# Kernel optimization log

Hardware: AMD Instinct MI355X
Metric: run time of the kernel (lower is better)

Reference implementation:

```python
import jax, jax.numpy as jnp
import numpy as np
from jax import lax

B, C, W, H = 32, 64, 32, 32
HEADS, RED = 4, 16
D = C // HEADS


def setup_inputs() -> dict:
    key = jax.random.key(0)
    ks = jax.random.split(key, 16)
    s = 0.05
    return {
        "x": jax.random.normal(ks[0], (B, C, W, H), jnp.float32),
        "Wq": jax.random.normal(ks[1], (C, C), jnp.float32) * s,
        "bq": jnp.zeros((C,), jnp.float32),
        "Wk": jax.random.normal(ks[2], (C, C), jnp.float32) * s,
        "bk": jnp.zeros((C,), jnp.float32),
        "Wv": jax.random.normal(ks[3], (C, C), jnp.float32) * s,
        "bv": jnp.zeros((C,), jnp.float32),
        "rel_h": jax.random.normal(ks[4], (1, HEADS, D, 1, H), jnp.float32),
        "rel_w": jax.random.normal(ks[5], (1, HEADS, D, W, 1), jnp.float32),
        "ln_g": jnp.ones((C, W, H), jnp.float32),
        "ln_b": jnp.zeros((C, W, H), jnp.float32),
        "ca_w1": jax.random.normal(ks[6], (C // RED, C), jnp.float32) * s,
        "ca_b1": jnp.zeros((C // RED,), jnp.float32),
        "ca_w2": jax.random.normal(ks[7], (C, C // RED), jnp.float32) * s,
        "ca_b2": jnp.zeros((C,), jnp.float32),
        "sa_w": jax.random.normal(ks[8], (1, 2, 7, 7), jnp.float32) * s,
        "sa_b": jnp.zeros((1,), jnp.float32),
    }


def reference(x, Wq, bq, Wk, bk, Wv, bv, rel_h, rel_w, ln_g, ln_b,
              ca_w1, ca_b1, ca_w2, ca_b2, sa_w, sa_b):
    b, c, w, h = x.shape
    n = w * h
    d = c // HEADS

    def conv1x1(t, wt, bt):
        return jnp.einsum('bchw,oc->bohw', t, wt) + bt[None, :, None, None]

    # ---- MHSA branch ----
    q = conv1x1(x, Wq, bq).reshape(b, HEADS, d, n)
    k = conv1x1(x, Wk, bk).reshape(b, HEADS, d, n)
    v = conv1x1(x, Wv, bv).reshape(b, HEADS, d, n)
    cc = jnp.einsum('bhdi,bhdj->bhij', q, k)                  # content-content
    pos = (rel_h + rel_w).reshape(1, HEADS, d, n)              # [1,H,d,N]
    cp = jnp.einsum('zhdi,bhdj->bhij', pos, q)                 # content-position
    att = jax.nn.softmax(cc + cp, axis=-1)                     # [b,H,N,N]
    out = jnp.einsum('bhdj,bhij->bhdi', v, att).reshape(b, c, w, h)
    # LayerNorm over (C,W,H)
    mu = jnp.mean(out, axis=(1, 2, 3), keepdims=True)
    var = jnp.var(out, axis=(1, 2, 3), keepdims=True)
    ln = (out - mu) * lax.rsqrt(var + 1e-5) * ln_g[None] + ln_b[None]
    mhsa = ln + x

    # ---- CBAM branch ----
    avg = jnp.mean(x, axis=(2, 3))                             # [b,c]
    mx = jnp.max(x, axis=(2, 3))

    def mlp(f):
        hid = jax.nn.relu(jnp.einsum('bc,oc->bo', f, ca_w1) + ca_b1)
        return jnp.einsum('bc,oc->bo', hid, ca_w2) + ca_b2

    ch_att = jax.nn.sigmoid(mlp(avg) + mlp(mx))[:, :, None, None]
    xc = ch_att * x
    feat = jnp.stack([jnp.mean(xc, axis=1), jnp.max(xc, axis=1)], axis=1)  # [b,2,w,h]
    sp = lax.conv_general_dilated(feat, sa_w, (1, 1), 'SAME',
                                  dimension_numbers=('NCHW', 'OIHW', 'NCHW'))
    sp = sp + sa_b[None, :, None, None]
    cbam = jax.nn.sigmoid(sp) * xc

    return mhsa + cbam + x
```

## Files before the change

### kernel.cpp

```cpp
#include <hip/hip_runtime.h>

#define BB 32
#define CC 64
#define WW 32
#define HHT 32
#define NH 4
#define DHD 16
#define NN 1024
#define LOG2E 1.4426950408889634f

typedef __attribute__((ext_vector_type(8))) short bf16x8;
typedef __attribute__((ext_vector_type(4))) float f32x4;

__device__ __forceinline__ float wave_sum(float v) {
#pragma unroll
  for (int off = 32; off > 0; off >>= 1) v += __shfl_down(v, off, 64);
  return v;
}
__device__ __forceinline__ float wave_max(float v) {
#pragma unroll
  for (int off = 32; off > 0; off >>= 1) v = fmaxf(v, __shfl_down(v, off, 64));
  return v;
}
__device__ __forceinline__ unsigned bf16pair(float lo, float hi) {
  unsigned a = __float_as_uint(lo), b = __float_as_uint(hi);
  a += 0x7FFFu + ((a >> 16) & 1u);
  b += 0x7FFFu + ((b >> 16) & 1u);
  return (a >> 16) | (b & 0xFFFF0000u);
}
__device__ __forceinline__ short bf16s(float f) {
  unsigned a = __float_as_uint(f);
  a += 0x7FFFu + ((a >> 16) & 1u);
  return (short)(a >> 16);
}

__global__ __launch_bounds__(256) void qkv_kernel(
    const float* __restrict__ x,
    const float* __restrict__ Wq, const float* __restrict__ bq,
    const float* __restrict__ Wk, const float* __restrict__ bk,
    const float* __restrict__ Wv, const float* __restrict__ bv,
    short* __restrict__ KQ, short* __restrict__ Vb, float* __restrict__ lnzero)
{
  __shared__ __align__(16) short Ws[192 * 72];
  const int tid = threadIdx.x;
  const int b = blockIdx.y, nt = blockIdx.x;

  if (tid < 192) {
    const int m = tid >> 4, dd = tid & 15;
    const int mat = m >> 2, h = m & 3;
    const float* src = (mat == 0 ? Wk : (mat == 1 ? Wq : Wv)) + (h * 16 + dd) * CC;
    const float scale = (mat == 0) ? LOG2E : 1.f;
    short* dst = Ws + tid * 72;
#pragma unroll
    for (int c8 = 0; c8 < 8; ++c8) {
      const float4 f0 = *reinterpret_cast<const float4*>(src + c8 * 8);
      const float4 f1 = *reinterpret_cast<const float4*>(src + c8 * 8 + 4);
      uint4 u;
      u.x = bf16pair(f0.x*scale, f0.y*scale); u.y = bf16pair(f0.z*scale, f0.w*scale);
      u.z = bf16pair(f1.x*scale, f1.y*scale); u.w = bf16pair(f1.z*scale, f1.w*scale);
      *reinterpret_cast<uint4*>(dst + c8 * 8) = u;
    }
  }
  if (blockIdx.x == 0 && blockIdx.y == 0 && tid < 64) lnzero[tid] = 0.f;
  __syncthreads();

  const int wid = tid >> 6, lane = tid & 63, Q = lane >> 4, il = lane & 15;
  const int n = nt * 64 + wid * 16 + il;
  const float* xb = x + (size_t)b * CC * NN;

  union { bf16x8 s; unsigned u[4]; } bfr[2];
#pragma unroll
  for (int half = 0; half < 2; ++half) {
#pragma unroll
    for (int p = 0; p < 4; ++p) {
      const int c0 = 32 * half + 8 * Q + 2 * p;
      const float f0 = xb[(size_t)c0 * NN + n];
      const float f1 = xb[(size_t)(c0 + 1) * NN + n];
      bfr[half].u[p] = bf16pair(f0, f1);
    }
  }

  const f32x4 zero4 = {0.f, 0.f, 0.f, 0.f};
  f32x4 acc[12];
#pragma unroll
  for (int m = 0; m < 12; ++m) {
    const short* wr = Ws + (m * 16 + il) * 72;
    const bf16x8 a0 = *reinterpret_cast<const bf16x8*>(wr + 8 * Q);
    const bf16x8 a1 = *reinterpret_cast<const bf16x8*>(wr + 32 + 8 * Q);
    acc[m] = __builtin_amdgcn_mfma_f32_16x16x32_bf16(a0, bfr[0].s, zero4, 0, 0, 0);
    acc[m] = __builtin_amdgcn_mfma_f32_16x16x32_bf16(a1, bfr[1].s, acc[m], 0, 0, 0);
  }

#pragma unroll
  for (int m = 0; m < 12; ++m) {
    const int mat = m >> 2, h = m & 3;
    const float bsc = (mat == 0) ? LOG2E : 1.f;
    const float4 bias = *reinterpret_cast<const float4*>(
        (mat == 0 ? bk : (mat == 1 ? bq : bv)) + h * 16 + 4 * Q);
    const float v0 = acc[m][0] + bias.x*bsc, v1 = acc[m][1] + bias.y*bsc;
    const float v2 = acc[m][2] + bias.z*bsc, v3 = acc[m][3] + bias.w*bsc;
    if (mat < 2) {
      uint2 pk;
      pk.x = bf16pair(v0, v1); pk.y = bf16pair(v2, v3);
      *reinterpret_cast<uint2*>(KQ + ((size_t)(b * NH + h) * NN + n) * 32 +
                                (mat == 0 ? 0 : 16) + 4 * Q) = pk;
    } else {
      short* vb = Vb + ((size_t)(b * NH + h) * 16 + 4 * Q) * NN + n;
      vb[0]            = bf16s(v0);
      vb[(size_t)NN]   = bf16s(v1);
      vb[2*(size_t)NN] = bf16s(v2);
      vb[3*(size_t)NN] = bf16s(v3);
    }
  }
}

__global__ __launch_bounds__(256, 4) void flash_kernel(
    const short* __restrict__ KQ, const short* __restrict__ Vb,
    const float* __restrict__ rel_h, const float* __restrict__ rel_w,
    float* __restrict__ attnout, float* __restrict__ lnsum, float* __restrict__ lnsum2)
{
  const int tid = threadIdx.x;
  const int wid = tid >> 6, lane = tid & 63;
  const int Q = lane >> 4, il = lane & 15;
  const int bh = blockIdx.x;
  const int h = bh & 3, b = bh >> 2;
  const int pr = wid & 1;
  const int jh = wid >> 1;
  const int ibase = blockIdx.y * 128 + pr * 64;
  const int j0base = jh * 512;

  bf16x8 bfrag[4];
#pragma unroll
  for (int g2 = 0; g2 < 4; ++g2) {
    const int i = ibase + g2*16 + il;
    if (Q < 2) {
      bfrag[g2] = *reinterpret_cast<const bf16x8*>(KQ + ((size_t)bh*NN + i)*32 + 16 + 8*Q);
    } else {
      const int wrow = i >> 5, hcol = i & 31;
      union { bf16x8 s; unsigned u[4]; } t;
#pragma unroll
      for (int p = 0; p < 4; ++p) {
        const int d0 = 8*(Q-2) + 2*p;
        const float f0 = LOG2E*(rel_h[(h*DHD + d0)*HHT + hcol] + rel_w[(h*DHD + d0)*WW + wrow]);
        const float f1 = LOG2E*(rel_h[(h*DHD + d0+1)*HHT + hcol] + rel_w[(h*DHD + d0+1)*WW + wrow]);
        t.u[p] = bf16pair(f0, f1);
      }
      bfrag[g2] = t.s;
    }
  }

  const short* KQb = KQ + (size_t)bh*NN*32;
  const short* Vbb = Vb + ((size_t)bh*16 + il)*NN;
  const f32x4 zero4 = {0.f, 0.f, 0.f, 0.f};
  f32x4 acc[4]  = {zero4, zero4, zero4, zero4};
  f32x4 lacc[4] = {zero4, zero4, zero4, zero4};
  union { bf16x8 s; unsigned u[4]; } ones;
  ones.u[0] = ones.u[1] = ones.u[2] = ones.u[3] = 0x3F803F80u;

#pragma unroll 2
  for (int t = 0; t < 8; ++t) {
    const int j0 = j0base + t*64;
    bf16x8 ag[4];
#pragma unroll
    for (int g = 0; g < 4; ++g)
      ag[g] = *reinterpret_cast<const bf16x8*>(KQb + (size_t)(j0 + 16*g + il)*32 + 8*Q);
    union { bf16x8 s; unsigned u[4]; } bv0, bv1;
    {
      const short* vp0 = Vbb + j0 + 4*Q;
      const uint2 l0 = *reinterpret_cast<const uint2*>(vp0);
      const uint2 h0 = *reinterpret_cast<const uint2*>(vp0 + 16);
      const uint2 l1 = *reinterpret_cast<const uint2*>(vp0 + 32);
      const uint2 h1 = *reinterpret_cast<const uint2*>(vp0 + 48);
      bv0.u[0] = l0.x; bv0.u[1] = l0.y; bv0.u[2] = h0.x; bv0.u[3] = h0.y;
      bv1.u[0] = l1.x; bv1.u[1] = l1.y; bv1.u[2] = h1.x; bv1.u[3] = h1.y;
    }

#pragma unroll
    for (int g2 = 0; g2 < 4; ++g2) {
      unsigned pk[4][2];
#pragma unroll
      for (int g = 0; g < 4; ++g) {
        const f32x4 s = __builtin_amdgcn_mfma_f32_16x16x32_bf16(ag[g], bfrag[g2], zero4, 0, 0, 0);
        const float p0 = __builtin_amdgcn_exp2f(s[0]);
        const float p1 = __builtin_amdgcn_exp2f(s[1]);
        const float p2 = __builtin_amdgcn_exp2f(s[2]);
        const float p3 = __builtin_amdgcn_exp2f(s[3]);
        pk[g][0] = bf16pair(p0, p1);
        pk[g][1] = bf16pair(p2, p3);
      }
#pragma unroll
      for (int hh = 0; hh < 2; ++hh) {
        union { bf16x8 s; unsigned u[4]; } ap;
        ap.u[0] = pk[2*hh][0];   ap.u[1] = pk[2*hh][1];
        ap.u[2] = pk[2*hh+1][0]; ap.u[3] = pk[2*hh+1][1];
        acc[g2]  = __builtin_amdgcn_mfma_f32_16x16x32_bf16(ap.s, hh ? bv1.s : bv0.s, acc[g2], 0, 0, 0);
        lacc[g2] = __builtin_amdgcn_mfma_f32_16x16x32_bf16(ap.s, ones.s, lacc[g2], 0, 0, 0);
      }
    }
  }

  __shared__ float cmb[2][32][64];
  __shared__ float r1[2], r2[2];
  if (jh == 1) {
#pragma unroll
    for (int g2 = 0; g2 < 4; ++g2)
#pragma unroll
      for (int r = 0; r < 4; ++r) {
        cmb[pr][g2*4 + r][lane]      = acc[g2][r];
        cmb[pr][16 + g2*4 + r][lane] = lacc[g2][r];
      }
  }
  __syncthreads();
  if (jh == 0) {
    float s1 = 0.f, s2 = 0.f;
#pragma unroll
    for (int g2 = 0; g2 < 4; ++g2)
#pragma unroll
      for (int r = 0; r < 4; ++r) {
        const float num = acc[g2][r]  + cmb[pr][g2*4 + r][lane];
        const float den = lacc[g2][r] + cmb[pr][16 + g2*4 + r][lane];
        const float v = num / den;
        const int ig = ibase + g2*16 + 4*Q + r;
        attnout[((size_t)b*CC + h*DHD + il)*NN + ig] = v;
        s1 += v; s2 += v*v;
      }
    s1 = wave_sum(s1); s2 = wave_sum(s2);
    if (lane == 0) { r1[pr] = s1; r2[pr] = s2; }
  }
  __syncthreads();
  if (tid == 0) {
    atomicAdd(&lnsum[b],  r1[0] + r1[1]);
    atomicAdd(&lnsum2[b], r2[0] + r2[1]);
  }
}

__global__ __launch_bounds__(256) void cbamstats_kernel(
    const float* __restrict__ x, float* __restrict__ avg, float* __restrict__ mx)
{
  const int bc = blockIdx.x, tid = threadIdx.x;
  const float* p = x + (size_t)bc*NN;
  float s = 0.f, m = -3.0e38f;
  for (int u = tid; u < NN; u += 256) { const float v = p[u]; s += v; m = fmaxf(m, v); }
  s = wave_sum(s); m = wave_max(m);
  __shared__ float rs[4], rm[4];
  const int wid = tid >> 6, lane = tid & 63;
  if (lane == 0) { rs[wid] = s; rm[wid] = m; }
  __syncthreads();
  if (tid == 0) {
    avg[bc] = (rs[0]+rs[1]+rs[2]+rs[3]) * (1.f/NN);
    mx[bc]  = fmaxf(fmaxf(rm[0], rm[1]), fmaxf(rm[2], rm[3]));
  }
}

__global__ __launch_bounds__(256) void mlpfeat_kernel(
    const float* __restrict__ x, const float* __restrict__ avg, const float* __restrict__ mxv,
    const float* __restrict__ w1, const float* __restrict__ b1,
    const float* __restrict__ w2, const float* __restrict__ b2,
    float* __restrict__ chv, float* __restrict__ feat)
{
  const int b = blockIdx.y, qq = blockIdx.x, tid = threadIdx.x;
  __shared__ float sa[CC], sm[CC], sch[CC];
  __shared__ float ps[4][64], pm[4][64];
  if (tid < CC) { sa[tid] = avg[b*CC + tid]; sm[tid] = mxv[b*CC + tid]; }
  __syncthreads();
  if (tid < CC) {
    float s = 2.f * b2[tid];
#pragma unroll
    for (int o = 0; o < 4; ++o) {
      float ha = b1[o], hm = b1[o];
#pragma unroll
      for (int k = 0; k < CC; ++k) { ha += w1[o*CC + k]*sa[k]; hm += w1[o*CC + k]*sm[k]; }
      s += w2[tid*4 + o] * (fmaxf(ha, 0.f) + fmaxf(hm, 0.f));
    }
    const float c = 1.f/(1.f + __expf(-s));
    sch[tid] = c;
    if (qq == 0) chv[b*CC + tid] = c;
  }
  __syncthreads();
  const int nl = tid & 63, cg = tid >> 6;
  const int n = qq*64 + nl;
  float s = 0.f, m = -3.0e38f;
#pragma unroll
  for (int c = cg*16; c < cg*16 + 16; ++c) {
    const float v = sch[c] * x[((size_t)b*CC + c)*NN + n];
    s += v; m = fmaxf(m, v);
  }
  ps[cg][nl] = s; pm[cg][nl] = m;
  __syncthreads();
  if (cg == 0) {
    const float S = ps[0][nl]+ps[1][nl]+ps[2][nl]+ps[3][nl];
    const float M = fmaxf(fmaxf(pm[0][nl], pm[1][nl]), fmaxf(pm[2][nl], pm[3][nl]));
    feat[(size_t)b*2*NN + n]      = S * (1.f/CC);
    feat[(size_t)b*2*NN + NN + n] = M;
  }
}

__global__ __launch_bounds__(256) void final_kernel(
    const float* __restrict__ x, const float* __restrict__ attn,
    const float* __restrict__ ln_g, const float* __restrict__ ln_b,
    const float* __restrict__ feat, const float* __restrict__ ch,
    const float* __restrict__ lnsum, const float* __restrict__ lnsum2,
    const float* __restrict__ sa_w, const float* __restrict__ sa_b,
    float* __restrict__ out)
{
  const int b = blockIdx.y;
  const int c0 = blockIdx.z * 16;
  const int n = blockIdx.x*256 + threadIdx.x;
  const int w = n >> 5, hh = n & 31;
  __shared__ float sch[CC];
  __shared__ float swt[98];
  if (threadIdx.x < CC) sch[threadIdx.x] = ch[b*CC + threadIdx.x];
  if (threadIdx.x < 98) swt[threadIdx.x] = sa_w[threadIdx.x];
  __syncthreads();

  float s = sa_b[0];
#pragma unroll
  for (int ci = 0; ci < 2; ++ci)
#pragma unroll
    for (int kh = 0; kh < 7; ++kh) {
      const int wy = w + kh - 3;
      if (wy < 0 || wy >= WW) continue;
#pragma unroll
      for (int kw = 0; kw < 7; ++kw) {
        const int hx = hh + kw - 3;
        if (hx < 0 || hx >= HHT) continue;
        s += feat[((size_t)(b*2) + ci)*NN + wy*HHT + hx] * swt[ci*49 + kh*7 + kw];
      }
    }
  const float sg = 1.f/(1.f + __expf(-s));
  const float inv = 1.f/(CC*NN);
  const float m = lnsum[b]*inv;
  const float var = lnsum2[b]*inv - m*m;
  const float r = rsqrtf(var + 1e-5f);
#pragma unroll
  for (int c = c0; c < c0 + 16; ++c) {
    const size_t idx = ((size_t)b*CC + c)*NN + n;
    const float xa = x[idx];
    const float ln = (attn[idx] - m) * r * ln_g[c*NN + n] + ln_b[c*NN + n];
    out[idx] = ln + 2.f*xa + sg * sch[c] * xa;
  }
}

extern "C" void kernel_launch(void* const* d_in, const int* in_sizes, int n_in,
                              void* d_out, int out_size, void* d_ws, size_t ws_size,
                              hipStream_t stream)
{
  const float* x     = (const float*)d_in[0];
  const float* Wq    = (const float*)d_in[1];
  const float* bq    = (const float*)d_in[2];
  const float* Wk    = (const float*)d_in[3];
  const float* bk    = (const float*)d_in[4];
  const float* Wv    = (const float*)d_in[5];
  const float* bv    = (const float*)d_in[6];
  const float* rel_h = (const float*)d_in[7];
  const float* rel_w = (const float*)d_in[8];
  const float* ln_g  = (const float*)d_in[9];
  const float* ln_b  = (const float*)d_in[10];
  const float* cw1   = (const float*)d_in[11];
  const float* cb1   = (const float*)d_in[12];
  const float* cw2   = (const float*)d_in[13];
  const float* cb2   = (const float*)d_in[14];
  const float* saw   = (const float*)d_in[15];
  const float* sab   = (const float*)d_in[16];
  float* out = (float*)d_out;

  short* KQ = (short*)d_ws;
  short* Vb = KQ + (size_t)128*1024*32;
  float* fs = (float*)(Vb + (size_t)128*16*1024);
  float* lnsum  = fs;
  float* lnsum2 = fs + 32;
  float* avg    = fs + 64;
  float* mxv    = avg + 2048;
  float* chv    = mxv + 2048;
  float* feat   = chv + 2048;
  float* attn   = out;

  qkv_kernel<<<dim3(16, BB), 256, 0, stream>>>(x, Wq, bq, Wk, bk, Wv, bv, KQ, Vb, lnsum);
  flash_kernel<<<dim3(BB*NH, 8), 256, 0, stream>>>(KQ, Vb, rel_h, rel_w, attn, lnsum, lnsum2);
  cbamstats_kernel<<<BB*CC, 256, 0, stream>>>(x, avg, mxv);
  mlpfeat_kernel<<<dim3(16, BB), 256, 0, stream>>>(x, avg, mxv, cw1, cb1, cw2, cb2, chv, feat);
  final_kernel<<<dim3(4, BB, 4), 256, 0, stream>>>(x, attn, ln_g, ln_b, feat, chv, lnsum, lnsum2, saw, sab, out);
}
```

Measured before the change: 161.4 us.

## Split flash attention keys four ways per block and use hardware bf16 pack

Each flash block now covers 64 query rows instead of 128, and its four waves each take a quarter of the key range rather than two waves per half. Partial numerators and denominators from waves 1-3 are combined through shared memory by wave 0, and the grid doubles to 2048 blocks. The block-level reduction of the layer-norm statistics is replaced by per-block atomics. Separately, the manual round-to-nearest bf16 packing is replaced by the HIP float2-to-bfloat162 intrinsic, which may map to a native conversion instruction. The finer split gives more parallelism and shorter key loops, at the cost of more shared-memory combine traffic and more redundant Q fragment setup.

```diff
diff --git a/kernel.cpp b/kernel.cpp
--- a/kernel.cpp
+++ b/kernel.cpp
@@ -1,4 +1,5 @@
 #include <hip/hip_runtime.h>
+#include <hip/hip_bf16.h>
 
 #define BB 32
 #define CC 64
@@ -22,11 +23,10 @@
   for (int off = 32; off > 0; off >>= 1) v = fmaxf(v, __shfl_down(v, off, 64));
   return v;
 }
-__device__ __forceinline__ unsigned bf16pair(float lo, float hi) {
-  unsigned a = __float_as_uint(lo), b = __float_as_uint(hi);
-  a += 0x7FFFu + ((a >> 16) & 1u);
-  b += 0x7FFFu + ((b >> 16) & 1u);
-  return (a >> 16) | (b & 0xFFFF0000u);
+__device__ __forceinline__ unsigned packbf2(float lo, float hi) {
+  union { __hip_bfloat162 h; unsigned u; } c;
+  c.h = __float22bfloat162_rn(float2{lo, hi});
+  return c.u;
 }
 __device__ __forceinline__ short bf16s(float f) {
   unsigned a = __float_as_uint(f);
@@ -56,8 +56,8 @@
       const float4 f0 = *reinterpret_cast<const float4*>(src + c8 * 8);
       const float4 f1 = *reinterpret_cast<const float4*>(src + c8 * 8 + 4);
       uint4 u;
-      u.x = bf16pair(f0.x*scale, f0.y*scale); u.y = bf16pair(f0.z*scale, f0.w*scale);
-      u.z = bf16pair(f1.x*scale, f1.y*scale); u.w = bf16pair(f1.z*scale, f1.w*scale);
+      u.x = packbf2(f0.x*scale, f0.y*scale); u.y = packbf2(f0.z*scale, f0.w*scale);
+      u.z = packbf2(f1.x*scale, f1.y*scale); u.w = packbf2(f1.z*scale, f1.w*scale);
       *reinterpret_cast<uint4*>(dst + c8 * 8) = u;
     }
   }
@@ -76,7 +76,7 @@
       const int c0 = 32 * half + 8 * Q + 2 * p;
       const float f0 = xb[(size_t)c0 * NN + n];
       const float f1 = xb[(size_t)(c0 + 1) * NN + n];
-      bfr[half].u[p] = bf16pair(f0, f1);
+      bfr[half].u[p] = packbf2(f0, f1);
     }
   }
 
@@ -101,7 +101,7 @@
     const float v2 = acc[m][2] + bias.z*bsc, v3 = acc[m][3] + bias.w*bsc;
     if (mat < 2) {
       uint2 pk;
-      pk.x = bf16pair(v0, v1); pk.y = bf16pair(v2, v3);
+      pk.x = packbf2(v0, v1); pk.y = packbf2(v2, v3);
       *reinterpret_cast<uint2*>(KQ + ((size_t)(b * NH + h) * NN + n) * 32 +
                                 (mat == 0 ? 0 : 16) + 4 * Q) = pk;
     } else {
@@ -124,10 +124,8 @@
   const int Q = lane >> 4, il = lane & 15;
   const int bh = blockIdx.x;
   const int h = bh & 3, b = bh >> 2;
-  const int pr = wid & 1;
-  const int jh = wid >> 1;
-  const int ibase = blockIdx.y * 128 + pr * 64;
-  const int j0base = jh * 512;
+  const int ibase = blockIdx.y * 64;
+  const int j0base = wid * 256;
 
   bf16x8 bfrag[4];
 #pragma unroll
@@ -143,7 +141,7 @@
         const int d0 = 8*(Q-2) + 2*p;
         const float f0 = LOG2E*(rel_h[(h*DHD + d0)*HHT + hcol] + rel_w[(h*DHD + d0)*WW + wrow]);
         const float f1 = LOG2E*(rel_h[(h*DHD + d0+1)*HHT + hcol] + rel_w[(h*DHD + d0+1)*WW + wrow]);
-        t.u[p] = bf16pair(f0, f1);
+        t.u[p] = packbf2(f0, f1);
       }
       bfrag[g2] = t.s;
     }
@@ -158,7 +156,7 @@
   ones.u[0] = ones.u[1] = ones.u[2] = ones.u[3] = 0x3F803F80u;
 
 #pragma unroll 2
-  for (int t = 0; t < 8; ++t) {
+  for (int t = 0; t < 4; ++t) {
     const int j0 = j0base + t*64;
     bf16x8 ag[4];
 #pragma unroll
@@ -185,8 +183,8 @@
         const float p1 = __builtin_amdgcn_exp2f(s[1]);
         const float p2 = __builtin_amdgcn_exp2f(s[2]);
         const float p3 = __builtin_amdgcn_exp2f(s[3]);
-        pk[g][0] = bf16pair(p0, p1);
-        pk[g][1] = bf16pair(p2, p3);
+        pk[g][0] = packbf2(p0, p1);
+        pk[g][1] = packbf2(p2, p3);
       }
 #pragma unroll
       for (int hh = 0; hh < 2; ++hh) {
@@ -199,38 +197,36 @@
     }
   }
 
-  __shared__ float cmb[2][32][64];
-  __shared__ float r1[2], r2[2];
-  if (jh == 1) {
+  __shared__ float cmb[3][32][64];
+  if (wid) {
 #pragma unroll
     for (int g2 = 0; g2 < 4; ++g2)
 #pragma unroll
       for (int r = 0; r < 4; ++r) {
-        cmb[pr][g2*4 + r][lane]      = acc[g2][r];
-        cmb[pr][16 + g2*4 + r][lane] = lacc[g2][r];
-      }
-  }
-  __syncthreads();
-  if (jh == 0) {
+        cmb[wid-1][g2*4 + r][lane]      = acc[g2][r];
+        cmb[wid-1][16 + g2*4 + r][lane] = lacc[g2][r];
+      }
+  }
+  __syncthreads();
+  if (wid == 0) {
     float s1 = 0.f, s2 = 0.f;
 #pragma unroll
     for (int g2 = 0; g2 < 4; ++g2)
 #pragma unroll
       for (int r = 0; r < 4; ++r) {
-        const float num = acc[g2][r]  + cmb[pr][g2*4 + r][lane];
-        const float den = lacc[g2][r] + cmb[pr][16 + g2*4 + r][lane];
+        float num = acc[g2][r], den = lacc[g2][r];
+#pragma unroll
+        for (int s = 0; s < 3; ++s) {
+          num += cmb[s][g2*4 + r][lane];
+          den += cmb[s][16 + g2*4 + r][lane];
+        }
         const float v = num / den;
         const int ig = ibase + g2*16 + 4*Q + r;
         attnout[((size_t)b*CC + h*DHD + il)*NN + ig] = v;
         s1 += v; s2 += v*v;
       }
     s1 = wave_sum(s1); s2 = wave_sum(s2);
-    if (lane == 0) { r1[pr] = s1; r2[pr] = s2; }
-  }
-  __syncthreads();
-  if (tid == 0) {
-    atomicAdd(&lnsum[b],  r1[0] + r1[1]);
-    atomicAdd(&lnsum2[b], r2[0] + r2[1]);
+    if (lane == 0) { atomicAdd(&lnsum[b], s1); atomicAdd(&lnsum2[b], s2); }
   }
 }
 
@@ -376,7 +372,7 @@
   float* attn   = out;
 
   qkv_kernel<<<dim3(16, BB), 256, 0, stream>>>(x, Wq, bq, Wk, bk, Wv, bv, KQ, Vb, lnsum);
-  flash_kernel<<<dim3(BB*NH, 8), 256, 0, stream>>>(KQ, Vb, rel_h, rel_w, attn, lnsum, lnsum2);
+  flash_kernel<<<dim3(BB*NH, 16), 256, 0, stream>>>(KQ, Vb, rel_h, rel_w, attn, lnsum, lnsum2);
   cbamstats_kernel<<<BB*CC, 256, 0, stream>>>(x, avg, mxv);
   mlpfeat_kernel<<<dim3(16, BB), 256, 0, stream>>>(x, avg, mxv, cw1, cb1, cw2, cb2, chv, feat);
   final_kernel<<<dim3(4, BB, 4), 256, 0, stream>>>(x, attn, ln_g, ln_b, feat, chv, lnsum, lnsum2, saw, sab, out);
```

Measured after the change: 173.0 us. +7.2%, slower.

## Software-pipeline flash attention loop with prefetch and skewed score MFMAs

Applied to the files above, without the earlier changes.

Restructures the flash kernel's inner loop so the score MFMAs for the next query group are issued before the exp/pack/PV MFMAs of the current group, and K/V tiles are double-buffered with a load issued two tiles ahead. The aim is to overlap global load latency and MFMA latency with the exp2 and bf16 packing ALU work. It also switches bf16 packing to the HIP intrinsic, vectorizes the output store to float4, and lowers the occupancy hint from 4 to 3 blocks per CU. The extra live registers for prefetched tiles and skewed scores reduce occupancy.

```diff
diff --git a/kernel.cpp b/kernel.cpp
--- a/kernel.cpp
+++ b/kernel.cpp
@@ -1,4 +1,5 @@
 #include <hip/hip_runtime.h>
+#include <hip/hip_bf16.h>
 
 #define BB 32
 #define CC 64
@@ -22,11 +23,10 @@
   for (int off = 32; off > 0; off >>= 1) v = fmaxf(v, __shfl_down(v, off, 64));
   return v;
 }
-__device__ __forceinline__ unsigned bf16pair(float lo, float hi) {
-  unsigned a = __float_as_uint(lo), b = __float_as_uint(hi);
-  a += 0x7FFFu + ((a >> 16) & 1u);
-  b += 0x7FFFu + ((b >> 16) & 1u);
-  return (a >> 16) | (b & 0xFFFF0000u);
+__device__ __forceinline__ unsigned packbf2(float lo, float hi) {
+  union { __hip_bfloat162 h; unsigned u; } c;
+  c.h = __float22bfloat162_rn(float2{lo, hi});
+  return c.u;
 }
 __device__ __forceinline__ short bf16s(float f) {
   unsigned a = __float_as_uint(f);
@@ -56,8 +56,8 @@
       const float4 f0 = *reinterpret_cast<const float4*>(src + c8 * 8);
       const float4 f1 = *reinterpret_cast<const float4*>(src + c8 * 8 + 4);
       uint4 u;
-      u.x = bf16pair(f0.x*scale, f0.y*scale); u.y = bf16pair(f0.z*scale, f0.w*scale);
-      u.z = bf16pair(f1.x*scale, f1.y*scale); u.w = bf16pair(f1.z*scale, f1.w*scale);
+      u.x = packbf2(f0.x*scale, f0.y*scale); u.y = packbf2(f0.z*scale, f0.w*scale);
+      u.z = packbf2(f1.x*scale, f1.y*scale); u.w = packbf2(f1.z*scale, f1.w*scale);
       *reinterpret_cast<uint4*>(dst + c8 * 8) = u;
     }
   }
@@ -76,7 +76,7 @@
       const int c0 = 32 * half + 8 * Q + 2 * p;
       const float f0 = xb[(size_t)c0 * NN + n];
       const float f1 = xb[(size_t)(c0 + 1) * NN + n];
-      bfr[half].u[p] = bf16pair(f0, f1);
+      bfr[half].u[p] = packbf2(f0, f1);
     }
   }
 
@@ -101,7 +101,7 @@
     const float v2 = acc[m][2] + bias.z*bsc, v3 = acc[m][3] + bias.w*bsc;
     if (mat < 2) {
       uint2 pk;
-      pk.x = bf16pair(v0, v1); pk.y = bf16pair(v2, v3);
+      pk.x = packbf2(v0, v1); pk.y = packbf2(v2, v3);
       *reinterpret_cast<uint2*>(KQ + ((size_t)(b * NH + h) * NN + n) * 32 +
                                 (mat == 0 ? 0 : 16) + 4 * Q) = pk;
     } else {
@@ -114,7 +114,7 @@
   }
 }
 
-__global__ __launch_bounds__(256, 4) void flash_kernel(
+__global__ __launch_bounds__(256, 3) void flash_kernel(
     const short* __restrict__ KQ, const short* __restrict__ Vb,
     const float* __restrict__ rel_h, const float* __restrict__ rel_w,
     float* __restrict__ attnout, float* __restrict__ lnsum, float* __restrict__ lnsum2)
@@ -143,7 +143,7 @@
         const int d0 = 8*(Q-2) + 2*p;
         const float f0 = LOG2E*(rel_h[(h*DHD + d0)*HHT + hcol] + rel_w[(h*DHD + d0)*WW + wrow]);
         const float f1 = LOG2E*(rel_h[(h*DHD + d0+1)*HHT + hcol] + rel_w[(h*DHD + d0+1)*WW + wrow]);
-        t.u[p] = bf16pair(f0, f1);
+        t.u[p] = packbf2(f0, f1);
       }
       bfrag[g2] = t.s;
     }
@@ -154,50 +154,89 @@
   const f32x4 zero4 = {0.f, 0.f, 0.f, 0.f};
   f32x4 acc[4]  = {zero4, zero4, zero4, zero4};
   f32x4 lacc[4] = {zero4, zero4, zero4, zero4};
-  union { bf16x8 s; unsigned u[4]; } ones;
+  union u32x4 { bf16x8 s; unsigned u[4]; };
+  u32x4 ones;
   ones.u[0] = ones.u[1] = ones.u[2] = ones.u[3] = 0x3F803F80u;
 
-#pragma unroll 2
+  bf16x8 agc[4], agn[4];
+  u32x4 bv0c, bv1c, bv0n, bv1n;
+
+#define LOADTILE(T, AG, BV0, BV1)                                              \
+  {                                                                            \
+    const int j0_ = j0base + ((T) & 7) * 64;                                   \
+    _Pragma("unroll")                                                          \
+    for (int g_ = 0; g_ < 4; ++g_)                                             \
+      AG[g_] = *reinterpret_cast<const bf16x8*>(                               \
+          KQb + (size_t)(j0_ + 16*g_ + il)*32 + 8*Q);                          \
+    const short* vp_ = Vbb + j0_ + 4*Q;                                        \
+    const uint2 l0_ = *reinterpret_cast<const uint2*>(vp_);                    \
+    const uint2 h0_ = *reinterpret_cast<const uint2*>(vp_ + 16);               \
+    const uint2 l1_ = *reinterpret_cast<const uint2*>(vp_ + 32);               \
+    const uint2 h1_ = *reinterpret_cast<const uint2*>(vp_ + 48);               \
+    BV0.u[0] = l0_.x; BV0.u[1] = l0_.y; BV0.u[2] = h0_.x; BV0.u[3] = h0_.y;    \
+    BV1.u[0] = l1_.x; BV1.u[1] = l1_.y; BV1.u[2] = h1_.x; BV1.u[3] = h1_.y;    \
+  }
+
+#define FINISH(GP, B0, B1)                                                     \
+  {                                                                            \
+    unsigned pk_[4][2];                                                        \
+    _Pragma("unroll")                                                          \
+    for (int g_ = 0; g_ < 4; ++g_) {                                           \
+      const float p0_ = __builtin_amdgcn_exp2f(sp[g_][0]);                     \
+      const float p1_ = __builtin_amdgcn_exp2f(sp[g_][1]);                     \
+      const float p2_ = __builtin_amdgcn_exp2f(sp[g_][2]);                     \
+      const float p3_ = __builtin_amdgcn_exp2f(sp[g_][3]);                     \
+      pk_[g_][0] = packbf2(p0_, p1_);                                          \
+      pk_[g_][1] = packbf2(p2_, p3_);                                          \
+    }                                                                          \
+    u32x4 ap0_, ap1_;                                                          \
+    ap0_.u[0] = pk_[0][0]; ap0_.u[1] = pk_[0][1];                              \
+    ap0_.u[2] = pk_[1][0]; ap0_.u[3] = pk_[1][1];                              \
+    ap1_.u[0] = pk_[2][0]; ap1_.u[1] = pk_[2][1];                              \
+    ap1_.u[2] = pk_[3][0]; ap1_.u[3] = pk_[3][1];                              \
+    acc[GP]  = __builtin_amdgcn_mfma_f32_16x16x32_bf16(ap0_.s, B0.s,  acc[GP], 0, 0, 0);  \
+    lacc[GP] = __builtin_amdgcn_mfma_f32_16x16x32_bf16(ap0_.s, ones.s, lacc[GP], 0, 0, 0);\
+    acc[GP]  = __builtin_amdgcn_mfma_f32_16x16x32_bf16(ap1_.s, B1.s,  acc[GP], 0, 0, 0);  \
+    lacc[GP] = __builtin_amdgcn_mfma_f32_16x16x32_bf16(ap1_.s, ones.s, lacc[GP], 0, 0, 0);\
+  }
+
+  LOADTILE(0, agc, bv0c, bv1c);
+  LOADTILE(1, agn, bv0n, bv1n);
+  f32x4 sp[4];
+#pragma unroll
+  for (int g = 0; g < 4; ++g)
+    sp[g] = __builtin_amdgcn_mfma_f32_16x16x32_bf16(agc[g], bfrag[0], zero4, 0, 0, 0);
+
   for (int t = 0; t < 8; ++t) {
-    const int j0 = j0base + t*64;
-    bf16x8 ag[4];
-#pragma unroll
-    for (int g = 0; g < 4; ++g)
-      ag[g] = *reinterpret_cast<const bf16x8*>(KQb + (size_t)(j0 + 16*g + il)*32 + 8*Q);
-    union { bf16x8 s; unsigned u[4]; } bv0, bv1;
-    {
-      const short* vp0 = Vbb + j0 + 4*Q;
-      const uint2 l0 = *reinterpret_cast<const uint2*>(vp0);
-      const uint2 h0 = *reinterpret_cast<const uint2*>(vp0 + 16);
-      const uint2 l1 = *reinterpret_cast<const uint2*>(vp0 + 32);
-      const uint2 h1 = *reinterpret_cast<const uint2*>(vp0 + 48);
-      bv0.u[0] = l0.x; bv0.u[1] = l0.y; bv0.u[2] = h0.x; bv0.u[3] = h0.y;
-      bv1.u[0] = l1.x; bv1.u[1] = l1.y; bv1.u[2] = h1.x; bv1.u[3] = h1.y;
-    }
-
-#pragma unroll
-    for (int g2 = 0; g2 < 4; ++g2) {
-      unsigned pk[4][2];
-#pragma unroll
-      for (int g = 0; g < 4; ++g) {
-        const f32x4 s = __builtin_amdgcn_mfma_f32_16x16x32_bf16(ag[g], bfrag[g2], zero4, 0, 0, 0);
-        const float p0 = __builtin_amdgcn_exp2f(s[0]);
-        const float p1 = __builtin_amdgcn_exp2f(s[1]);
-        const float p2 = __builtin_amdgcn_exp2f(s[2]);
-        const float p3 = __builtin_amdgcn_exp2f(s[3]);
-        pk[g][0] = bf16pair(p0, p1);
-        pk[g][1] = bf16pair(p2, p3);
-      }
-#pragma unroll
-      for (int hh = 0; hh < 2; ++hh) {
-        union { bf16x8 s; unsigned u[4]; } ap;
-        ap.u[0] = pk[2*hh][0];   ap.u[1] = pk[2*hh][1];
-        ap.u[2] = pk[2*hh+1][0]; ap.u[3] = pk[2*hh+1][1];
-        acc[g2]  = __builtin_amdgcn_mfma_f32_16x16x32_bf16(ap.s, hh ? bv1.s : bv0.s, acc[g2], 0, 0, 0);
-        lacc[g2] = __builtin_amdgcn_mfma_f32_16x16x32_bf16(ap.s, ones.s, lacc[g2], 0, 0, 0);
-      }
-    }
-  }
+#pragma unroll
+    for (int g2 = 1; g2 < 4; ++g2) {
+      f32x4 sn[4];
+#pragma unroll
+      for (int g = 0; g < 4; ++g)
+        sn[g] = __builtin_amdgcn_mfma_f32_16x16x32_bf16(agc[g], bfrag[g2], zero4, 0, 0, 0);
+      FINISH(g2 - 1, bv0c, bv1c);
+#pragma unroll
+      for (int g = 0; g < 4; ++g) sp[g] = sn[g];
+    }
+    if (t < 7) {
+      u32x4 b0o = bv0c, b1o = bv1c;
+#pragma unroll
+      for (int g = 0; g < 4; ++g) agc[g] = agn[g];
+      bv0c = bv0n; bv1c = bv1n;
+      f32x4 sn[4];
+#pragma unroll
+      for (int g = 0; g < 4; ++g)
+        sn[g] = __builtin_amdgcn_mfma_f32_16x16x32_bf16(agc[g], bfrag[0], zero4, 0, 0, 0);
+      FINISH(3, b0o, b1o);
+#pragma unroll
+      for (int g = 0; g < 4; ++g) sp[g] = sn[g];
+      LOADTILE(t + 2, agn, bv0n, bv1n);
+    } else {
+      FINISH(3, bv0c, bv1c);
+    }
+  }
+#undef LOADTILE
+#undef FINISH
 
   __shared__ float cmb[2][32][64];
   __shared__ float r1[2], r2[2];
@@ -214,16 +253,20 @@
   if (jh == 0) {
     float s1 = 0.f, s2 = 0.f;
 #pragma unroll
-    for (int g2 = 0; g2 < 4; ++g2)
+    for (int g2 = 0; g2 < 4; ++g2) {
+      float4 vv;
+      float* vp = &vv.x;
 #pragma unroll
       for (int r = 0; r < 4; ++r) {
         const float num = acc[g2][r]  + cmb[pr][g2*4 + r][lane];
         const float den = lacc[g2][r] + cmb[pr][16 + g2*4 + r][lane];
         const float v = num / den;
-        const int ig = ibase + g2*16 + 4*Q + r;
-        attnout[((size_t)b*CC + h*DHD + il)*NN + ig] = v;
+        vp[r] = v;
         s1 += v; s2 += v*v;
       }
+      *reinterpret_cast<float4*>(
+          &attnout[((size_t)b*CC + h*DHD + il)*NN + ibase + g2*16 + 4*Q]) = vv;
+    }
     s1 = wave_sum(s1); s2 = wave_sum(s2);
     if (lane == 0) { r1[pr] = s1; r2[pr] = s2; }
   }
```

New measurement: 165.0 us. 2.3% more time.
